# Optimization experiments

Measured on AMD Instinct MI355X. Metric: run time of the kernel, lower is better.

## Reference

```python
import jax, jax.numpy as jnp
import numpy as np

N = 400000      # total atoms across batch of molecules
E = 1600000     # directed edges (avg degree 4)
G = 4096        # number of graphs (molecules)
F_IN = 78       # atomic feature size
H = 128         # gnn hidden dims (gnn_0 = gnn_1 = 128)
FF0, FF1 = 256, 128


def _lin(k, fan_in, fan_out):
    return jax.random.normal(k, (fan_in, fan_out), jnp.float32) / np.sqrt(fan_in).astype(np.float32)


def setup_inputs() -> dict:
    key = jax.random.key(0)
    ks = jax.random.split(key, 10)
    x = jax.random.normal(ks[0], (N, F_IN), jnp.float32)
    edge_index = jax.random.randint(ks[1], (2, E), 0, N, dtype=jnp.int64)
    # sorted graph ids, guaranteed non-empty segments (empty segment -> -inf under max pool)
    batch = (jnp.arange(N, dtype=jnp.int64) * G) // N
    return {
        'x': x, 'edge_index': edge_index, 'batch': batch,
        'W0': _lin(ks[2], F_IN, H), 'b0': jnp.zeros((H,), jnp.float32),
        'W1': _lin(ks[3], H, H),    'b1': jnp.zeros((H,), jnp.float32),
        'Wf0': _lin(ks[4], H, FF0), 'bf0': jnp.zeros((FF0,), jnp.float32),
        'Wf1': _lin(ks[5], FF0, FF1), 'bf1': jnp.zeros((FF1,), jnp.float32),
    }


def _gcn_conv(h, W, b, src, dst, dinv):
    # GCNConv with add_self_loops=True, symmetric normalization.
    hw = h @ W                                     # [N, out]
    norm = dinv[src] * dinv[dst]                   # [E]
    msg = hw[src] * norm[:, None]                  # gather + scale
    agg = jax.ops.segment_sum(msg, dst, num_segments=h.shape[0])
    agg = agg + hw * (dinv * dinv)[:, None]        # self-loop contribution
    return agg + b


def reference(x, edge_index, batch, W0, b0, W1, b1, Wf0, bf0, Wf1, bf1):
    src, dst = edge_index[0], edge_index[1]
    # degree of A + I computed at target nodes (PyG gcn_norm uses col)
    deg = jax.ops.segment_sum(jnp.ones((E,), x.dtype), dst, num_segments=N) + 1.0
    dinv = jax.lax.rsqrt(deg)

    h = jax.nn.relu(_gcn_conv(x, W0, b0, src, dst, dinv))
    h = jax.nn.relu(_gcn_conv(h, W1, b1, src, dst, dinv))

    g = jax.ops.segment_max(h, batch, num_segments=G)   # global max pool [G, H]

    g = jax.nn.relu(g @ Wf0 + bf0)   # dropout is identity in eval
    g = jax.nn.relu(g @ Wf1 + bf1)
    return g
```

## Files before the change

kernel.cpp:

```cpp
#include <hip/hip_runtime.h>
#include <cstdint>
#include <cstddef>

#define NATOMS 400000
#define NEDGES 1600000
#define NGRAPH 4096
#define F_INN  78
#define HDIM   128
#define FF0D   256
#define FF1D   128

#define XPAD   80

typedef __attribute__((ext_vector_type(8))) short short8;
typedef __attribute__((ext_vector_type(4))) short short4v;
typedef __attribute__((ext_vector_type(4))) float f32x4;
typedef __attribute__((ext_vector_type(2))) float f32x2;

static __device__ __forceinline__ short f2bf(float f) {
    unsigned u = __builtin_bit_cast(unsigned, f);
    unsigned r = (u + 0x7fffu + ((u >> 16) & 1u)) >> 16;
    return (short)r;
}
static __device__ __forceinline__ float bf2f(unsigned short u) {
    return __builtin_bit_cast(float, ((unsigned)u) << 16);
}

__global__ __launch_bounds__(256) void k_degi(const int* __restrict__ dst,
                                              int* __restrict__ deg,
                                              int* __restrict__ rank, int E) {
    int e = blockIdx.x * 256 + threadIdx.x;
    if (e < E) rank[e] = atomicAdd(&deg[dst[e]], 1);
}

__global__ __launch_bounds__(256) void k_scan1(int* __restrict__ data,
                                               int* __restrict__ blockSums,
                                               float* __restrict__ dinv, int n) {
    __shared__ int ts[256];
    const int base = blockIdx.x * 1024 + threadIdx.x * 4;
    int v[4];
    #pragma unroll
    for (int j = 0; j < 4; ++j) v[j] = (base + j < n) ? data[base + j] : 0;
    #pragma unroll
    for (int j = 0; j < 4; ++j)
        if (base + j < n) dinv[base + j] = rsqrtf((float)v[j] + 1.0f);
    const int tot = v[0] + v[1] + v[2] + v[3];
    ts[threadIdx.x] = tot;
    __syncthreads();
    #pragma unroll
    for (int off = 1; off < 256; off <<= 1) {
        int t = (threadIdx.x >= off) ? ts[threadIdx.x - off] : 0;
        __syncthreads();
        ts[threadIdx.x] += t;
        __syncthreads();
    }
    int run = ts[threadIdx.x] - tot;
    #pragma unroll
    for (int j = 0; j < 4; ++j) {
        if (base + j < n) data[base + j] = run;
        run += v[j];
    }
    if (threadIdx.x == 255) blockSums[blockIdx.x] = ts[255];
}

__global__ __launch_bounds__(512) void k_scan2(int* __restrict__ blockSums, int nb) {
    __shared__ int ts[512];
    int v = (threadIdx.x < nb) ? blockSums[threadIdx.x] : 0;
    ts[threadIdx.x] = v;
    __syncthreads();
    #pragma unroll
    for (int off = 1; off < 512; off <<= 1) {
        int t = (threadIdx.x >= off) ? ts[threadIdx.x - off] : 0;
        __syncthreads();
        ts[threadIdx.x] += t;
        __syncthreads();
    }
    if (threadIdx.x < nb) blockSums[threadIdx.x] = ts[threadIdx.x] - v;
}

__global__ __launch_bounds__(256) void k_scan3(int* __restrict__ data,
                                               const int* __restrict__ blockSums,
                                               int n, int total) {
    const int off = blockSums[blockIdx.x];
    const int base = blockIdx.x * 1024 + threadIdx.x * 4;
    #pragma unroll
    for (int j = 0; j < 4; ++j)
        if (base + j < n) data[base + j] += off;
    if (blockIdx.x == 0 && threadIdx.x == 0) data[n] = total;
}

__global__ __launch_bounds__(256) void k_fill(const int* __restrict__ src,
                                              const int* __restrict__ dst,
                                              const int* __restrict__ row_start,
                                              const int* __restrict__ rank,
                                              int2* __restrict__ csr_ev,
                                              const float* __restrict__ dinv, int E) {
    int e = blockIdx.x * 256 + threadIdx.x;
    if (e >= E) return;
    int d = dst[e];
    int s = src[e];
    int pos = row_start[d] + rank[e];
    float norm = dinv[s] * dinv[d];
    csr_ev[pos] = make_int2(s, __builtin_bit_cast(int, norm));
}

template<int KC, int KSRC, bool BIASROW>
__global__ __launch_bounds__(64) void k_packw(const float* __restrict__ W,
                                              const float* __restrict__ b,
                                              short* __restrict__ wf) {
    int t = blockIdx.x * 64 + threadIdx.x;
    int f = t >> 6, lane = t & 63;
    int ct = f / KC, kc = f % KC;
    int n  = ct * 16 + (lane & 15);
    int k0 = kc * 32 + (lane >> 4) * 8;
    short8 o;
    #pragma unroll
    for (int j = 0; j < 8; ++j) {
        int k = k0 + j;
        float v = 0.f;
        if (k < KSRC) v = W[(size_t)k * 128 + n];
        else if (BIASROW && k == KSRC) v = b[n];
        o[j] = f2bf(v);
    }
    *(short8*)(wf + (size_t)t * 8) = o;
}

__global__ __launch_bounds__(256) void k_packx(const float* __restrict__ x,
                                               unsigned short* __restrict__ xb) {
    int t = blockIdx.x * 256 + threadIdx.x;
    if (t >= NATOMS * 20) return;
    int n = t / 20, g = t % 20;
    const float* xr = x + (size_t)n * F_INN + g * 4;
    short4v o;
    if (g < 19) {
        f32x2 a = *(const f32x2*)(xr);
        f32x2 b = *(const f32x2*)(xr + 2);
        o.x = f2bf(a.x); o.y = f2bf(a.y); o.z = f2bf(b.x); o.w = f2bf(b.y);
    } else {
        f32x2 a = *(const f32x2*)(xr);
        o.x = f2bf(a.x); o.y = f2bf(a.y); o.z = 0; o.w = 0;
    }
    *(short4v*)(xb + (size_t)n * XPAD + g * 4) = o;
}

__global__ __launch_bounds__(256) void k_fused0(
    const unsigned short* __restrict__ xb, const short* __restrict__ wfrag,
    const int* __restrict__ row_start, const int2* __restrict__ csr_ev,
    const float* __restrict__ dinv, short* __restrict__ outp)
{
    constexpr int XLDS = 104;
    __shared__ __align__(16) short lds_w[24 * 64 * 8];
    __shared__ __align__(16) unsigned short xs[32 * XLDS];
    __shared__ __align__(16) char lds_st[4 * 2048];

    const int tid = threadIdx.x;
    #pragma unroll
    for (int it = 0; it < 6; ++it) {
        int t = it * 256 + tid;
        *(short8*)(lds_w + (size_t)t * 8) = *(const short8*)(wfrag + (size_t)t * 8);
    }

    {
        const int nl = tid >> 3;
        const int n  = blockIdx.x * 32 + nl;
        const int l  = tid & 7;
        const int c8 = l * 8;
        const int ct = 64 + l * 2;
        const float dv = dinv[n];
        const float d2 = dv * dv;

        float acc[8], tacc0, tacc1;
        {
            const short8 sv = *(const short8*)(xb + (size_t)n * XPAD + c8);
            const unsigned tv = *(const unsigned*)(xb + (size_t)n * XPAD + ct);
            #pragma unroll
            for (int j = 0; j < 8; ++j) acc[j] = bf2f((unsigned short)sv[j]) * d2;
            tacc0 = bf2f((unsigned short)(tv & 0xffff)) * d2;
            tacc1 = bf2f((unsigned short)(tv >> 16)) * d2;
        }

        const int s0 = row_start[n], s1 = row_start[n + 1];
        int i = s0;
        for (; i + 3 < s1; i += 4) {
            const int2 e0 = csr_ev[i];
            const int2 e1 = csr_ev[i + 1];
            const int2 e2 = csr_ev[i + 2];
            const int2 e3 = csr_ev[i + 3];
            const short8 r0 = *(const short8*)(xb + (size_t)e0.x * XPAD + c8);
            const short8 r1 = *(const short8*)(xb + (size_t)e1.x * XPAD + c8);
            const short8 r2 = *(const short8*)(xb + (size_t)e2.x * XPAD + c8);
            const short8 r3 = *(const short8*)(xb + (size_t)e3.x * XPAD + c8);
            const unsigned t0 = *(const unsigned*)(xb + (size_t)e0.x * XPAD + ct);
            const unsigned t1 = *(const unsigned*)(xb + (size_t)e1.x * XPAD + ct);
            const unsigned t2 = *(const unsigned*)(xb + (size_t)e2.x * XPAD + ct);
            const unsigned t3 = *(const unsigned*)(xb + (size_t)e3.x * XPAD + ct);
            const float w0 = __builtin_bit_cast(float, e0.y);
            const float w1 = __builtin_bit_cast(float, e1.y);
            const float w2 = __builtin_bit_cast(float, e2.y);
            const float w3 = __builtin_bit_cast(float, e3.y);
            #pragma unroll
            for (int j = 0; j < 8; ++j) acc[j] = fmaf(bf2f((unsigned short)r0[j]), w0, acc[j]);
            #pragma unroll
            for (int j = 0; j < 8; ++j) acc[j] = fmaf(bf2f((unsigned short)r1[j]), w1, acc[j]);
            #pragma unroll
            for (int j = 0; j < 8; ++j) acc[j] = fmaf(bf2f((unsigned short)r2[j]), w2, acc[j]);
            #pragma unroll
            for (int j = 0; j < 8; ++j) acc[j] = fmaf(bf2f((unsigned short)r3[j]), w3, acc[j]);
            tacc0 = fmaf(bf2f((unsigned short)(t0 & 0xffff)), w0, tacc0);
            tacc1 = fmaf(bf2f((unsigned short)(t0 >> 16)),    w0, tacc1);
            tacc0 = fmaf(bf2f((unsigned short)(t1 & 0xffff)), w1, tacc0);
            tacc1 = fmaf(bf2f((unsigned short)(t1 >> 16)),    w1, tacc1);
            tacc0 = fmaf(bf2f((unsigned short)(t2 & 0xffff)), w2, tacc0);
            tacc1 = fmaf(bf2f((unsigned short)(t2 >> 16)),    w2, tacc1);
            tacc0 = fmaf(bf2f((unsigned short)(t3 & 0xffff)), w3, tacc0);
            tacc1 = fmaf(bf2f((unsigned short)(t3 >> 16)),    w3, tacc1);
        }
        for (; i < s1; ++i) {
            const int2 e0 = csr_ev[i];
            const short8 r0 = *(const short8*)(xb + (size_t)e0.x * XPAD + c8);
            const unsigned t0 = *(const unsigned*)(xb + (size_t)e0.x * XPAD + ct);
            const float w0 = __builtin_bit_cast(float, e0.y);
            #pragma unroll
            for (int j = 0; j < 8; ++j) acc[j] = fmaf(bf2f((unsigned short)r0[j]), w0, acc[j]);
            tacc0 = fmaf(bf2f((unsigned short)(t0 & 0xffff)), w0, tacc0);
            tacc1 = fmaf(bf2f((unsigned short)(t0 >> 16)),    w0, tacc1);
        }

        short8 o;
        #pragma unroll
        for (int j = 0; j < 8; ++j) o[j] = f2bf(acc[j]);
        *(short8*)(xs + nl * XLDS + c8) = o;
        unsigned to;
        if (l == 7) to = 0x00003F80u;
        else {
            to = (unsigned)(unsigned short)f2bf(tacc0) |
                 ((unsigned)(unsigned short)f2bf(tacc1) << 16);
        }
        *(unsigned*)(xs + nl * XLDS + ct) = to;
        *(unsigned*)(xs + nl * XLDS + 80 + l * 2) = 0u;
    }
    __syncthreads();

    const int lane = tid & 63;
    const int wid  = tid >> 6;
    const int m = lane & 15, q = lane >> 4;
    const int T  = wid >> 1;
    const int c0 = (wid & 1) * 4;

    short8 afr[3];
    #pragma unroll
    for (int kc = 0; kc < 3; ++kc)
        afr[kc] = *(const short8*)(xs + (T * 16 + m) * XLDS + kc * 32 + q * 8);

    f32x4 acc[4];
    #pragma unroll
    for (int cc = 0; cc < 4; ++cc) acc[cc] = (f32x4){0.f, 0.f, 0.f, 0.f};
    #pragma unroll
    for (int kc = 0; kc < 3; ++kc)
        #pragma unroll
        for (int cc = 0; cc < 4; ++cc) {
            const short8 wv = *(const short8*)(lds_w + ((size_t)(((c0 + cc) * 3 + kc) * 64 + lane)) * 8);
            acc[cc] = __builtin_amdgcn_mfma_f32_16x16x32_bf16(wv, afr[kc], acc[cc], 0, 0, 0);
        }

    char* const st = lds_st + wid * 2048;
    #pragma unroll
    for (int cc = 0; cc < 4; ++cc) {
        short4v o;
        o.x = f2bf(fmaxf(acc[cc][0], 0.f));
        o.y = f2bf(fmaxf(acc[cc][1], 0.f));
        o.z = f2bf(fmaxf(acc[cc][2], 0.f));
        o.w = f2bf(fmaxf(acc[cc][3], 0.f));
        const int c = (cc * 32 + q * 8) ^ ((m & 7) << 4);
        *(short4v*)(st + m * 128 + c) = o;
    }
    #pragma unroll
    for (int p = 0; p < 2; ++p) {
        const int r  = p * 8 + (lane >> 3);
        const int cb = ((lane & 7) * 16) ^ ((r & 7) << 4);
        const short8 v = *(const short8*)(st + r * 128 + cb);
        *(short8*)(outp + (size_t)(blockIdx.x * 32 + T * 16 + r) * 128
                        + c0 * 16 + (lane & 7) * 8) = v;
    }
}

__global__ __launch_bounds__(512) void k_fused1(
    const unsigned short* __restrict__ hw, const short* __restrict__ wfrag,
    const int* __restrict__ row_start, const int2* __restrict__ csr_ev,
    const float* __restrict__ dinv, const float* __restrict__ bias,
    const int* __restrict__ batch, int* __restrict__ pool)
{
    constexpr int XL = 136;
    __shared__ __align__(16) short lds_w[32 * 64 * 8];
    __shared__ __align__(16) unsigned short xs[64 * XL];

    const int tid = threadIdx.x;
    #pragma unroll
    for (int it = 0; it < 4; ++it) {
        int t = it * 512 + tid;
        *(short8*)(lds_w + (size_t)t * 8) = *(const short8*)(wfrag + (size_t)t * 8);
    }

    {
        const int nl = tid >> 3;
        const int n  = blockIdx.x * 64 + nl;
        const int l  = tid & 7;
        const int cA = l * 8;
        const int cB = 64 + l * 8;
        const float dv = dinv[n];
        const float d2 = dv * dv;

        float aA[8], aB[8];
        {
            const short8 sa = *(const short8*)(hw + (size_t)n * HDIM + cA);
            const short8 sb = *(const short8*)(hw + (size_t)n * HDIM + cB);
            #pragma unroll
            for (int j = 0; j < 8; ++j) {
                aA[j] = bf2f((unsigned short)sa[j]) * d2;
                aB[j] = bf2f((unsigned short)sb[j]) * d2;
            }
        }

        const int s0 = row_start[n], s1 = row_start[n + 1];
        int i = s0;
        for (; i + 1 < s1; i += 2) {
            const int2 e0 = csr_ev[i];
            const int2 e1 = csr_ev[i + 1];
            const short8 rA0 = *(const short8*)(hw + (size_t)e0.x * HDIM + cA);
            const short8 rB0 = *(const short8*)(hw + (size_t)e0.x * HDIM + cB);
            const short8 rA1 = *(const short8*)(hw + (size_t)e1.x * HDIM + cA);
            const short8 rB1 = *(const short8*)(hw + (size_t)e1.x * HDIM + cB);
            const float w0 = __builtin_bit_cast(float, e0.y);
            const float w1 = __builtin_bit_cast(float, e1.y);
            #pragma unroll
            for (int j = 0; j < 8; ++j) {
                aA[j] = fmaf(bf2f((unsigned short)rA0[j]), w0, aA[j]);
                aB[j] = fmaf(bf2f((unsigned short)rB0[j]), w0, aB[j]);
            }
            #pragma unroll
            for (int j = 0; j < 8; ++j) {
                aA[j] = fmaf(bf2f((unsigned short)rA1[j]), w1, aA[j]);
                aB[j] = fmaf(bf2f((unsigned short)rB1[j]), w1, aB[j]);
            }
        }
        for (; i < s1; ++i) {
            const int2 e0 = csr_ev[i];
            const short8 rA0 = *(const short8*)(hw + (size_t)e0.x * HDIM + cA);
            const short8 rB0 = *(const short8*)(hw + (size_t)e0.x * HDIM + cB);
            const float w0 = __builtin_bit_cast(float, e0.y);
            #pragma unroll
            for (int j = 0; j < 8; ++j) {
                aA[j] = fmaf(bf2f((unsigned short)rA0[j]), w0, aA[j]);
                aB[j] = fmaf(bf2f((unsigned short)rB0[j]), w0, aB[j]);
            }
        }

        short8 oA, oB;
        #pragma unroll
        for (int j = 0; j < 8; ++j) { oA[j] = f2bf(aA[j]); oB[j] = f2bf(aB[j]); }
        *(short8*)(xs + nl * XL + cA) = oA;
        *(short8*)(xs + nl * XL + cB) = oB;
    }
    __syncthreads();

    const int lane = tid & 63;
    const int wid  = tid >> 6;
    const int m = lane & 15, q = lane >> 4;
    const int T  = wid >> 1;
    const int c0 = (wid & 1) * 4;

    short8 afr[4];
    #pragma unroll
    for (int kc = 0; kc < 4; ++kc)
        afr[kc] = *(const short8*)(xs + (T * 16 + m) * XL + kc * 32 + q * 8);

    f32x4 acc[4];
    #pragma unroll
    for (int cc = 0; cc < 4; ++cc) acc[cc] = (f32x4){0.f, 0.f, 0.f, 0.f};
    #pragma unroll
    for (int kc = 0; kc < 4; ++kc)
        #pragma unroll
        for (int cc = 0; cc < 4; ++cc) {
            const short8 wv = *(const short8*)(lds_w + ((size_t)(((c0 + cc) * 4 + kc) * 64 + lane)) * 8);
            acc[cc] = __builtin_amdgcn_mfma_f32_16x16x32_bf16(wv, afr[kc], acc[cc], 0, 0, 0);
        }

    const int nb    = blockIdx.x * 64;
    const int gbase = batch[nb];
    const int glast = batch[nb + 63];
    const int idx   = batch[nb + T * 16 + m] - gbase;

    float v[16];
    #pragma unroll
    for (int cc = 0; cc < 4; ++cc) {
        const f32x4 b4 = *(const f32x4*)(bias + (c0 + cc) * 16 + q * 4);
        #pragma unroll
        for (int j = 0; j < 4; ++j)
            v[cc * 4 + j] = fmaxf(acc[cc][j] + b4[j], 0.f);
    }

    {
        float r[16];
        #pragma unroll
        for (int k = 0; k < 16; ++k) r[k] = (idx == 0) ? v[k] : 0.f;
        #pragma unroll
        for (int msk = 1; msk <= 8; msk <<= 1)
            #pragma unroll
            for (int k = 0; k < 16; ++k)
                r[k] = fmaxf(r[k], __shfl_xor(r[k], msk));
        if (m == 0) {
            #pragma unroll
            for (int cc = 0; cc < 4; ++cc)
                #pragma unroll
                for (int j = 0; j < 4; ++j)
                    atomicMax(pool + (size_t)gbase * HDIM + (c0 + cc) * 16 + q * 4 + j,
                              __builtin_bit_cast(int, r[cc * 4 + j]));
        }
    }
    if (glast != gbase) {
        float r[16];
        #pragma unroll
        for (int k = 0; k < 16; ++k) r[k] = (idx == 1) ? v[k] : 0.f;
        #pragma unroll
        for (int msk = 1; msk <= 8; msk <<= 1)
            #pragma unroll
            for (int k = 0; k < 16; ++k)
                r[k] = fmaxf(r[k], __shfl_xor(r[k], msk));
        if (m == 0) {
            #pragma unroll
            for (int cc = 0; cc < 4; ++cc)
                #pragma unroll
                for (int j = 0; j < 4; ++j)
                    atomicMax(pool + (size_t)(gbase + 1) * HDIM + (c0 + cc) * 16 + q * 4 + j,
                              __builtin_bit_cast(int, r[cc * 4 + j]));
        }
    }
}

template<int K, int NC, bool OUT_RELU_BIAS>
__global__ __launch_bounds__(256) void k_gemm(
    const float* __restrict__ in, const float* __restrict__ W,
    const float* __restrict__ out_bias, float* __restrict__ out0, int M)
{
    constexpr int BK = 32;
    constexpr int TC = NC / 8;
    constexpr int TR = 256 / TC;
    constexpr int ROWS = TR * 8;
    constexpr int XST = ROWS + 4;

    __shared__ float xs[BK][XST];
    __shared__ float ws[BK][NC];

    const int tid = threadIdx.x;
    const int tc  = tid % TC;
    const int tr  = tid / TC;
    const int row0 = blockIdx.x * ROWS;

    float acc[8][8];
    #pragma unroll
    for (int i = 0; i < 8; ++i)
        #pragma unroll
        for (int j = 0; j < 8; ++j) acc[i][j] = 0.f;

    for (int k0 = 0; k0 < K; k0 += BK) {
        {
            constexpr int TASKS = BK * NC / 4;
            #pragma unroll
            for (int it = 0; it < TASKS / 256; ++it) {
                int t  = it * 256 + tid;
                int wk = t / (NC / 4);
                int wc = (t % (NC / 4)) * 4;
                *(float4*)(&ws[wk][wc]) = *(const float4*)(W + (size_t)(k0 + wk) * NC + wc);
            }
        }
        {
            constexpr int TASKS = ROWS * BK / 4;
            #pragma unroll
            for (int it = 0; it < TASKS / 256; ++it) {
                int t   = it * 256 + tid;
                int r   = t / (BK / 4);
                int kq  = (t % (BK / 4)) * 4;
                float4 x4 = *(const float4*)(in + (size_t)(row0 + r) * K + k0 + kq);
                xs[kq + 0][r] = x4.x; xs[kq + 1][r] = x4.y;
                xs[kq + 2][r] = x4.z; xs[kq + 3][r] = x4.w;
            }
        }
        __syncthreads();
        #pragma unroll 8
        for (int kk = 0; kk < BK; ++kk) {
            float a[8], b[8];
            #pragma unroll
            for (int i = 0; i < 8; ++i) a[i] = xs[kk][tr * 8 + i];
            #pragma unroll
            for (int j = 0; j < 8; ++j) b[j] = ws[kk][tc * 8 + j];
            #pragma unroll
            for (int i = 0; i < 8; ++i)
                #pragma unroll
                for (int j = 0; j < 8; ++j)
                    acc[i][j] = fmaf(a[i], b[j], acc[i][j]);
        }
        __syncthreads();
    }

    #pragma unroll
    for (int i = 0; i < 8; ++i) {
        const int row = row0 + tr * 8 + i;
        #pragma unroll
        for (int jq = 0; jq < 2; ++jq) {
            const int col = tc * 8 + jq * 4;
            float4 v;
            v.x = acc[i][jq * 4 + 0]; v.y = acc[i][jq * 4 + 1];
            v.z = acc[i][jq * 4 + 2]; v.w = acc[i][jq * 4 + 3];
            if constexpr (OUT_RELU_BIAS) {
                const float4 bb = *(const float4*)(out_bias + col);
                v.x = fmaxf(v.x + bb.x, 0.f); v.y = fmaxf(v.y + bb.y, 0.f);
                v.z = fmaxf(v.z + bb.z, 0.f); v.w = fmaxf(v.w + bb.w, 0.f);
            }
            *(float4*)(out0 + (size_t)row * NC + col) = v;
        }
    }
}

extern "C" void kernel_launch(void* const* d_in, const int* in_sizes, int n_in,
                              void* d_out, int out_size, void* d_ws, size_t ws_size,
                              hipStream_t stream) {
    const float* x    = (const float*)d_in[0];
    const int*   ei   = (const int*)d_in[1];
    const int*   batch= (const int*)d_in[2];
    const float* W0   = (const float*)d_in[3];
    const float* b0   = (const float*)d_in[4];
    const float* W1   = (const float*)d_in[5];
    const float* b1   = (const float*)d_in[6];
    const float* Wf0  = (const float*)d_in[7];
    const float* bf0  = (const float*)d_in[8];
    const float* Wf1  = (const float*)d_in[9];
    const float* bf1  = (const float*)d_in[10];
    float* out = (float*)d_out;

    const int* srcI = ei;
    const int* dstI = ei + NEDGES;

    constexpr int SCAN_NBLK = (NATOMS + 1023) / 1024;

    char* base = (char*)d_ws;
    int*   rank      = (int*)(base + 0);
    unsigned short* aggB = (unsigned short*)(base + 102400000);
    float* dinv      = (float*)(base + 204800000);
    int*   row_start = (int*)(base + 206400000);
    int2*  csr_ev    = (int2*)(base + 208000064);
    int*   blockSums = (int*)(base + 220800064);
    float* pool      = (float*)(base + 220802112);
    float* ff0       = (float*)(base + 222899264);
    short* wf0       = (short*)(base + 227093568);
    short* wf1       = (short*)(base + 227118144);
    unsigned short* xb = (unsigned short*)(base + 227150912);

    hipMemsetAsync(row_start, 0, (size_t)(NATOMS + 1) * sizeof(int), stream);
    hipMemsetAsync(pool, 0, (size_t)NGRAPH * HDIM * sizeof(float), stream);
    k_degi<<<(NEDGES + 255) / 256, 256, 0, stream>>>(dstI, row_start, rank, NEDGES);
    k_scan1<<<SCAN_NBLK, 256, 0, stream>>>(row_start, blockSums, dinv, NATOMS);
    k_scan2<<<1, 512, 0, stream>>>(blockSums, SCAN_NBLK);
    k_scan3<<<SCAN_NBLK, 256, 0, stream>>>(row_start, blockSums, NATOMS, NEDGES);
    k_fill<<<(NEDGES + 255) / 256, 256, 0, stream>>>(srcI, dstI, row_start, rank,
                                                     csr_ev, dinv, NEDGES);

    k_packw<3, F_INN, true><<<8 * 3, 64, 0, stream>>>(W0, b0, wf0);
    k_packw<4, HDIM, false><<<8 * 4, 64, 0, stream>>>(W1, nullptr, wf1);
    k_packx<<<(NATOMS * 20 + 255) / 256, 256, 0, stream>>>(x, xb);

    k_fused0<<<NATOMS / 32, 256, 0, stream>>>(xb, wf0, row_start, csr_ev, dinv,
                                              (short*)aggB);

    k_fused1<<<NATOMS / 64, 512, 0, stream>>>(aggB, wf1, row_start, csr_ev,
                                              dinv, b1, batch, (int*)pool);

    k_gemm<HDIM, FF0D, true><<<NGRAPH / 64, 256, 0, stream>>>(pool, Wf0, bf0, ff0, NGRAPH);
    k_gemm<FF0D, FF1D, true><<<NGRAPH / 128, 256, 0, stream>>>(ff0, Wf1, bf1, out, NGRAPH);
}
```

Measured before the change: 641.1 us.

## Split fused layer-1 aggregation into two column halves interleaved with MFMA

The fused second-layer kernel now gathers neighbour features one 64-column half at a time. Each half goes into a smaller LDS staging buffer (stride 72 instead of 136), and the MFMA K-chunks for that half run before the next half is gathered. The edge loop is unrolled by four instead of two. This is meant to cut register and LDS pressure and to keep more gathers in flight, at the cost of walking the CSR edge list twice and adding extra barriers.

```diff
diff --git a/kernel.cpp b/kernel.cpp
--- a/kernel.cpp
+++ b/kernel.cpp
@@ -290,7 +290,7 @@
     const float* __restrict__ dinv, const float* __restrict__ bias,
     const int* __restrict__ batch, int* __restrict__ pool)
 {
-    constexpr int XL = 136;
+    constexpr int XL = 72;
     __shared__ __align__(16) short lds_w[32 * 64 * 8];
     __shared__ __align__(16) unsigned short xs[64 * XL];
 
@@ -301,67 +301,12 @@
         *(short8*)(lds_w + (size_t)t * 8) = *(const short8*)(wfrag + (size_t)t * 8);
     }
 
-    {
-        const int nl = tid >> 3;
-        const int n  = blockIdx.x * 64 + nl;
-        const int l  = tid & 7;
-        const int cA = l * 8;
-        const int cB = 64 + l * 8;
-        const float dv = dinv[n];
-        const float d2 = dv * dv;
-
-        float aA[8], aB[8];
-        {
-            const short8 sa = *(const short8*)(hw + (size_t)n * HDIM + cA);
-            const short8 sb = *(const short8*)(hw + (size_t)n * HDIM + cB);
-            #pragma unroll
-            for (int j = 0; j < 8; ++j) {
-                aA[j] = bf2f((unsigned short)sa[j]) * d2;
-                aB[j] = bf2f((unsigned short)sb[j]) * d2;
-            }
-        }
-
-        const int s0 = row_start[n], s1 = row_start[n + 1];
-        int i = s0;
-        for (; i + 1 < s1; i += 2) {
-            const int2 e0 = csr_ev[i];
-            const int2 e1 = csr_ev[i + 1];
-            const short8 rA0 = *(const short8*)(hw + (size_t)e0.x * HDIM + cA);
-            const short8 rB0 = *(const short8*)(hw + (size_t)e0.x * HDIM + cB);
-            const short8 rA1 = *(const short8*)(hw + (size_t)e1.x * HDIM + cA);
-            const short8 rB1 = *(const short8*)(hw + (size_t)e1.x * HDIM + cB);
-            const float w0 = __builtin_bit_cast(float, e0.y);
-            const float w1 = __builtin_bit_cast(float, e1.y);
-            #pragma unroll
-            for (int j = 0; j < 8; ++j) {
-                aA[j] = fmaf(bf2f((unsigned short)rA0[j]), w0, aA[j]);
-                aB[j] = fmaf(bf2f((unsigned short)rB0[j]), w0, aB[j]);
-            }
-            #pragma unroll
-            for (int j = 0; j < 8; ++j) {
-                aA[j] = fmaf(bf2f((unsigned short)rA1[j]), w1, aA[j]);
-                aB[j] = fmaf(bf2f((unsigned short)rB1[j]), w1, aB[j]);
-            }
-        }
-        for (; i < s1; ++i) {
-            const int2 e0 = csr_ev[i];
-            const short8 rA0 = *(const short8*)(hw + (size_t)e0.x * HDIM + cA);
-            const short8 rB0 = *(const short8*)(hw + (size_t)e0.x * HDIM + cB);
-            const float w0 = __builtin_bit_cast(float, e0.y);
-            #pragma unroll
-            for (int j = 0; j < 8; ++j) {
-                aA[j] = fmaf(bf2f((unsigned short)rA0[j]), w0, aA[j]);
-                aB[j] = fmaf(bf2f((unsigned short)rB0[j]), w0, aB[j]);
-            }
-        }
-
-        short8 oA, oB;
-        #pragma unroll
-        for (int j = 0; j < 8; ++j) { oA[j] = f2bf(aA[j]); oB[j] = f2bf(aB[j]); }
-        *(short8*)(xs + nl * XL + cA) = oA;
-        *(short8*)(xs + nl * XL + cB) = oB;
-    }
-    __syncthreads();
+    const int nl = tid >> 3;
+    const int n  = blockIdx.x * 64 + nl;
+    const int l  = tid & 7;
+    const float dv = dinv[n];
+    const float d2 = dv * dv;
+    const int s0 = row_start[n], s1 = row_start[n + 1];
 
     const int lane = tid & 63;
     const int wid  = tid >> 6;
@@ -369,21 +314,70 @@
     const int T  = wid >> 1;
     const int c0 = (wid & 1) * 4;
 
-    short8 afr[4];
-    #pragma unroll
-    for (int kc = 0; kc < 4; ++kc)
-        afr[kc] = *(const short8*)(xs + (T * 16 + m) * XL + kc * 32 + q * 8);
-
     f32x4 acc[4];
     #pragma unroll
     for (int cc = 0; cc < 4; ++cc) acc[cc] = (f32x4){0.f, 0.f, 0.f, 0.f};
-    #pragma unroll
-    for (int kc = 0; kc < 4; ++kc)
-        #pragma unroll
-        for (int cc = 0; cc < 4; ++cc) {
-            const short8 wv = *(const short8*)(lds_w + ((size_t)(((c0 + cc) * 4 + kc) * 64 + lane)) * 8);
-            acc[cc] = __builtin_amdgcn_mfma_f32_16x16x32_bf16(wv, afr[kc], acc[cc], 0, 0, 0);
-        }
+
+    #pragma unroll
+    for (int half = 0; half < 2; ++half) {
+        const int cb = half * 64 + l * 8;
+
+        float a[8];
+        {
+            const short8 sv = *(const short8*)(hw + (size_t)n * HDIM + cb);
+            #pragma unroll
+            for (int j = 0; j < 8; ++j) a[j] = bf2f((unsigned short)sv[j]) * d2;
+        }
+        int i = s0;
+        for (; i + 3 < s1; i += 4) {
+            const int2 e0 = csr_ev[i];
+            const int2 e1 = csr_ev[i + 1];
+            const int2 e2 = csr_ev[i + 2];
+            const int2 e3 = csr_ev[i + 3];
+            const short8 r0 = *(const short8*)(hw + (size_t)e0.x * HDIM + cb);
+            const short8 r1 = *(const short8*)(hw + (size_t)e1.x * HDIM + cb);
+            const short8 r2 = *(const short8*)(hw + (size_t)e2.x * HDIM + cb);
+            const short8 r3 = *(const short8*)(hw + (size_t)e3.x * HDIM + cb);
+            const float w0 = __builtin_bit_cast(float, e0.y);
+            const float w1 = __builtin_bit_cast(float, e1.y);
+            const float w2 = __builtin_bit_cast(float, e2.y);
+            const float w3 = __builtin_bit_cast(float, e3.y);
+            #pragma unroll
+            for (int j = 0; j < 8; ++j) a[j] = fmaf(bf2f((unsigned short)r0[j]), w0, a[j]);
+            #pragma unroll
+            for (int j = 0; j < 8; ++j) a[j] = fmaf(bf2f((unsigned short)r1[j]), w1, a[j]);
+            #pragma unroll
+            for (int j = 0; j < 8; ++j) a[j] = fmaf(bf2f((unsigned short)r2[j]), w2, a[j]);
+            #pragma unroll
+            for (int j = 0; j < 8; ++j) a[j] = fmaf(bf2f((unsigned short)r3[j]), w3, a[j]);
+        }
+        for (; i < s1; ++i) {
+            const int2 e0 = csr_ev[i];
+            const short8 r0 = *(const short8*)(hw + (size_t)e0.x * HDIM + cb);
+            const float w0 = __builtin_bit_cast(float, e0.y);
+            #pragma unroll
+            for (int j = 0; j < 8; ++j) a[j] = fmaf(bf2f((unsigned short)r0[j]), w0, a[j]);
+        }
+
+        short8 o;
+        #pragma unroll
+        for (int j = 0; j < 8; ++j) o[j] = f2bf(a[j]);
+
+        if (half == 1) __syncthreads();
+        *(short8*)(xs + nl * XL + l * 8) = o;
+        __syncthreads();
+
+        #pragma unroll
+        for (int kc2 = 0; kc2 < 2; ++kc2) {
+            const short8 afr = *(const short8*)(xs + (T * 16 + m) * XL + kc2 * 32 + q * 8);
+            #pragma unroll
+            for (int cc = 0; cc < 4; ++cc) {
+                const short8 wv = *(const short8*)(lds_w +
+                    ((size_t)(((c0 + cc) * 4 + half * 2 + kc2) * 64 + lane)) * 8);
+                acc[cc] = __builtin_amdgcn_mfma_f32_16x16x32_bf16(wv, afr, acc[cc], 0, 0, 0);
+            }
+        }
+    }
 
     const int nb    = blockIdx.x * 64;
     const int gbase = batch[nb];
```

Result: slower. 661.0 us (+3.1%).
